# Kernel optimization log

Hardware: AMD Instinct MI355X
Metric: run time of the kernel (lower is better)

Reference implementation:

```python
import jax, jax.numpy as jnp
import numpy as np

SCALES = (3, 9, 17, 33)  # must be odd so padding=s//2 preserves spatial size


def _box_conv(img, s):
    # img: [B,1,H,W]; conv with an all-ones s x s kernel, 'same' padding for odd s
    k = jnp.ones((1, 1, s, s), img.dtype)
    p = s // 2
    return jax.lax.conv_general_dilated(
        img, k, window_strides=(1, 1), padding=[(p, p), (p, p)],
        dimension_numbers=("NCHW", "OIHW", "NCHW"))


def setup_inputs() -> dict:
    key = jax.random.key(0)
    B, C, H, W = 8, 3, 1024, 1024
    x = jax.random.normal(key, (B, C, H, W), dtype=jnp.float32)
    # mimicking sparse path-traced samples
    keep = jax.random.uniform(jax.random.fold_in(key, 1), (B, 1, H, W)) >= 0.3
    x = jnp.where(keep, x, 0.0)
    return {"x": x}


def reference(x):
    # F.conv2d(x, ones(1,3,1,1)/3) == per-pixel mean over the 3 channels
    lum = jnp.mean(x, axis=1, keepdims=True)          # [B,1,H,W]
    nonzero = (lum != 0).astype(lum.dtype)            # [B,1,H,W]
    feats = []
    for s in SCALES:
        count = _box_conv(nonzero, s)                 # number of nonzero pixels in window
        pool = _box_conv(lum, s) / jnp.maximum(count, 1.0)  # mean over nonzero pixels
        feats.append(count / float(s * s))            # percentage of nonzero pixels
        feats.append(pool)
    return jnp.concatenate(feats, axis=1)             # [B, 2*len(SCALES), H, W]
```

## Files before the change

### kernel.cpp

```cpp
#include <hip/hip_runtime.h>


constexpr int THREADS = 256;
constexpr int LOADW   = 256;
constexpr int HALO    = 17;
constexpr int COUT    = 223;
constexpr int RING    = 36;
constexpr int ROWSEG  = 64;

__device__ __forceinline__ void barrier_lds() {
    asm volatile("s_waitcnt lgkmcnt(0)" ::: "memory");
    __builtin_amdgcn_s_barrier();
    __builtin_amdgcn_sched_barrier(0);
}

template<int CTRL, int RM>
__device__ __forceinline__ float dppadd(float v) {
    int sh = __builtin_amdgcn_update_dpp(0, __float_as_int(v), CTRL, RM, 0xF, true);
    return v + __int_as_float(sh);
}

__device__ __forceinline__ float wave_iscan(float v) {
    v = dppadd<0x111, 0xF>(v);
    v = dppadd<0x112, 0xF>(v);
    v = dppadd<0x114, 0xF>(v);
    v = dppadd<0x118, 0xF>(v);
    v = dppadd<0x142, 0xA>(v);
    v = dppadd<0x143, 0xC>(v);
    return v;
}

__global__ __launch_bounds__(THREADS, 3)
void nzfeat_kernel(const float* __restrict__ x, float* __restrict__ out,
                   int B, int H, int W) {
    constexpr int   PP[4]   = {1, 4, 8, 16};
    constexpr float INVA[4] = {1.f/9.f, 1.f/81.f, 1.f/289.f, 1.f/1089.f};

    __shared__ float         ringL[RING][LOADW];
    __shared__ unsigned char ringN[RING][LOADW];
    __shared__ float2        wsum[2][4];

    const int t    = threadIdx.x;
    const int lane = t & 63;
    const int wv   = t >> 6;

    const int x0 = blockIdx.x * COUT;
    const int y0 = blockIdx.y * ROWSEG;
    const int b  = blockIdx.z;

    const int    gx   = x0 - HALO + t;
    const bool   gxok = (gx >= 0) && (gx < W);
    const int    gxc  = min(max(gx, 0), W - 1);
    const size_t HW   = (size_t)H * W;
    const float* xb   = x + (size_t)b * 3 * HW + gxc;

    auto load_row = [&](int r, float& a0, float& a1, float& a2) {
        const int rc = min(max(r, 0), H - 1);
        const float* p = xb + (size_t)rc * W;
        a0 = p[0]; a1 = p[HW]; a2 = p[2 * HW];
    };

    auto slotOf = [&](int r) { return (int)((unsigned)(r + 72) % (unsigned)RING); };
    auto wpos   = [&](int v) { return v >= RING ? v - RING : v; };
    auto wneg   = [&](int v) { return v < 0 ? v + RING : v; };

    auto scan_local = [&](float c0, float c1, float c2, int r, int which) -> float2 {
        float lum = 0.f;
        if (gxok && (unsigned)r < (unsigned)H)
            lum = (c0 + c1 + c2) * (1.0f / 3.0f);
        const bool nzb = (lum != 0.f);
        unsigned long long m = __ballot(nzb);
        int below = __builtin_amdgcn_mbcnt_hi((unsigned)(m >> 32),
                      __builtin_amdgcn_mbcnt_lo((unsigned)m, 0));
        float np = (float)below + (nzb ? 1.f : 0.f);
        float lp = wave_iscan(lum);
        if (lane == 63) wsum[which][wv] = make_float2(lp, np);
        return make_float2(lp, np);
    };

    auto combine_write = [&](float2 A, float2 Bv, int sA, int sB) {
        float oAl = 0.f, oAn = 0.f, oBl = 0.f, oBn = 0.f;
        #pragma unroll
        for (int w2 = 0; w2 < 3; ++w2)
            if (w2 < wv) {
                float2 u = wsum[0][w2]; float2 v = wsum[1][w2];
                oAl += u.x; oAn += u.y; oBl += v.x; oBn += v.y;
            }
        ringL[sA][t] = A.x + oAl;
        ringN[sA][t] = (unsigned char)(int)(A.y + oAn);
        ringL[sB][t] = Bv.x + oBl;
        ringN[sB][t] = (unsigned char)(int)(Bv.y + oBn);
    };

    float a0, a1, a2, b0c, b1c, b2c;
    load_row(y0 - 18, a0, a1, a2);
    load_row(y0 - 17, b0c, b1c, b2c);
    for (int i = 0; i < 17; ++i) {
        const int rA = y0 - 18 + 2 * i;
        float n0, n1, n2, m0, m1, m2;
        load_row(rA + 2, n0, n1, n2);
        load_row(rA + 3, m0, m1, m2);
        float2 A  = scan_local(a0, a1, a2, rA, 0);
        float2 Bv = scan_local(b0c, b1c, b2c, rA + 1, 1);
        barrier_lds();
        combine_write(A, Bv, slotOf(rA), slotOf(rA + 1));
        barrier_lds();
        a0 = n0; a1 = n1; a2 = n2; b0c = m0; b1c = m1; b2c = m2;
    }

    const bool activeCol = (t < COUT) && (x0 + t < W);
    float* outb = out + (size_t)b * 8 * HW + (x0 + t);

    float vl[4], vn[4];
    #pragma unroll
    for (int i = 0; i < 4; ++i) {
        const int p  = PP[i];
        const int d  = 2 * p + 1;
        const int x1 = t + HALO - p - 1;
        float sl = 0.f, sn = 0.f;
        for (int rr = y0 - 1 - p; rr <= y0 - 1 + p; ++rr) {
            const int s = slotOf(rr);
            sl += ringL[s][x1 + d] - ringL[s][x1];
            sn += (float)(unsigned char)(ringN[s][x1 + d] - ringN[s][x1]);
        }
        vl[i] = sl; vn[i] = sn;
    }

    int sy = slotOf(y0);
    for (int k = 0; k < ROWSEG / 2; ++k) {
        const int yk = y0 + 2 * k;
        const int wA = yk + 16;

        float n0, n1, n2, m0, m1, m2;
        load_row(wA + 2, n0, n1, n2);
        load_row(wA + 3, m0, m1, m2);

        float2 A  = scan_local(a0, a1, a2, wA, 0);
        float2 Bv = scan_local(b0c, b1c, b2c, wA + 1, 1);
        barrier_lds();
        combine_write(A, Bv, wpos(sy + 16), wpos(sy + 17));
        barrier_lds();

        #pragma unroll
        for (int i = 0; i < 4; ++i) {
            const int p  = PP[i];
            const int d  = 2 * p + 1;
            const int x1 = t + HALO - p - 1;
            const int sE = wpos(sy + p);
            const int sL = wneg(sy - 1 - p);
            const float hlE = ringL[sE][x1 + d] - ringL[sE][x1];
            const float hnE = (float)(unsigned char)(ringN[sE][x1 + d] - ringN[sE][x1]);
            const float hlL = ringL[sL][x1 + d] - ringL[sL][x1];
            const float hnL = (float)(unsigned char)(ringN[sL][x1 + d] - ringN[sL][x1]);
            vl[i] += hlE - hlL;
            vn[i] += hnE - hnL;
        }
        if (activeCol && yk < H) {
            float* o = outb + (size_t)yk * W;
            #pragma unroll
            for (int i = 0; i < 4; ++i) {
                o[(size_t)(2 * i) * HW]     = vn[i] * INVA[i];
                o[(size_t)(2 * i + 1) * HW] = vl[i] / fmaxf(vn[i], 1.f);
            }
        }

        #pragma unroll
        for (int i = 0; i < 4; ++i) {
            const int p  = PP[i];
            const int d  = 2 * p + 1;
            const int x1 = t + HALO - p - 1;
            const int sE = wpos(sy + p + 1);
            const int sL = wneg(sy - p);
            const float hlE = ringL[sE][x1 + d] - ringL[sE][x1];
            const float hnE = (float)(unsigned char)(ringN[sE][x1 + d] - ringN[sE][x1]);
            const float hlL = ringL[sL][x1 + d] - ringL[sL][x1];
            const float hnL = (float)(unsigned char)(ringN[sL][x1 + d] - ringN[sL][x1]);
            vl[i] += hlE - hlL;
            vn[i] += hnE - hnL;
        }
        if (activeCol && yk + 1 < H) {
            float* o = outb + (size_t)(yk + 1) * W;
            #pragma unroll
            for (int i = 0; i < 4; ++i) {
                o[(size_t)(2 * i) * HW]     = vn[i] * INVA[i];
                o[(size_t)(2 * i + 1) * HW] = vl[i] / fmaxf(vn[i], 1.f);
            }
        }

        sy = wpos(sy + 2);
        a0 = n0; a1 = n1; a2 = n2; b0c = m0; b1c = m1; b2c = m2;
    }
}

extern "C" void kernel_launch(void* const* d_in, const int* in_sizes, int n_in,
                              void* d_out, int out_size, void* d_ws, size_t ws_size,
                              hipStream_t stream) {
    const float* x   = (const float*)d_in[0];
    float*       out = (float*)d_out;

    const int H = 1024, W = 1024;
    const int B = in_sizes[0] / (3 * H * W);

    dim3 grid((W + COUT - 1) / COUT, (H + ROWSEG - 1) / ROWSEG, B);
    nzfeat_kernel<<<grid, dim3(THREADS), 0, stream>>>(x, out, B, H, W);
}
```

Measured before the change: 128.7 us.

## Skew scan and box-sum phases to drop one barrier per row pair

The ring buffer grows from 36 to 38 slots and the per-wave partial sums are double-buffered by parity. This lets the prefix-scan write for the next row pair happen in the same barrier interval as the box-sum reads of the previous pair, removing the second barrier in both loops. The main loop gains an extra drain iteration and extra conditionals. The pool division is also replaced with a hardware reciprocal multiply, which is slightly less accurate.

```diff
diff --git a/kernel.cpp b/kernel.cpp
--- a/kernel.cpp
+++ b/kernel.cpp
@@ -5,7 +5,7 @@
 constexpr int LOADW   = 256;
 constexpr int HALO    = 17;
 constexpr int COUT    = 223;
-constexpr int RING    = 36;
+constexpr int RING    = 38;
 constexpr int ROWSEG  = 64;
 
 __device__ __forceinline__ void barrier_lds() {
@@ -38,7 +38,7 @@
 
     __shared__ float         ringL[RING][LOADW];
     __shared__ unsigned char ringN[RING][LOADW];
-    __shared__ float2        wsum[2][4];
+    __shared__ float2        wsum[2][2][4];
 
     const int t    = threadIdx.x;
     const int lane = t & 63;
@@ -60,11 +60,11 @@
         a0 = p[0]; a1 = p[HW]; a2 = p[2 * HW];
     };
 
-    auto slotOf = [&](int r) { return (int)((unsigned)(r + 72) % (unsigned)RING); };
+    auto slotOf = [&](int r) { return (int)((unsigned)(r + 2 * RING) % (unsigned)RING); };
     auto wpos   = [&](int v) { return v >= RING ? v - RING : v; };
     auto wneg   = [&](int v) { return v < 0 ? v + RING : v; };
 
-    auto scan_local = [&](float c0, float c1, float c2, int r, int which) -> float2 {
+    auto scan_local = [&](float c0, float c1, float c2, int r, int par, int which) -> float2 {
         float lum = 0.f;
         if (gxok && (unsigned)r < (unsigned)H)
             lum = (c0 + c1 + c2) * (1.0f / 3.0f);
@@ -74,16 +74,16 @@
                       __builtin_amdgcn_mbcnt_lo((unsigned)m, 0));
         float np = (float)below + (nzb ? 1.f : 0.f);
         float lp = wave_iscan(lum);
-        if (lane == 63) wsum[which][wv] = make_float2(lp, np);
+        if (lane == 63) wsum[par][which][wv] = make_float2(lp, np);
         return make_float2(lp, np);
     };
 
-    auto combine_write = [&](float2 A, float2 Bv, int sA, int sB) {
+    auto combine_write = [&](int par, float2 A, float2 Bv, int sA, int sB) {
         float oAl = 0.f, oAn = 0.f, oBl = 0.f, oBn = 0.f;
         #pragma unroll
         for (int w2 = 0; w2 < 3; ++w2)
             if (w2 < wv) {
-                float2 u = wsum[0][w2]; float2 v = wsum[1][w2];
+                float2 u = wsum[par][0][w2]; float2 v = wsum[par][1][w2];
                 oAl += u.x; oAn += u.y; oBl += v.x; oBn += v.y;
             }
         ringL[sA][t] = A.x + oAl;
@@ -100,13 +100,13 @@
         float n0, n1, n2, m0, m1, m2;
         load_row(rA + 2, n0, n1, n2);
         load_row(rA + 3, m0, m1, m2);
-        float2 A  = scan_local(a0, a1, a2, rA, 0);
-        float2 Bv = scan_local(b0c, b1c, b2c, rA + 1, 1);
+        float2 A  = scan_local(a0, a1, a2, rA, i & 1, 0);
+        float2 Bv = scan_local(b0c, b1c, b2c, rA + 1, i & 1, 1);
         barrier_lds();
-        combine_write(A, Bv, slotOf(rA), slotOf(rA + 1));
-        barrier_lds();
+        combine_write(i & 1, A, Bv, slotOf(rA), slotOf(rA + 1));
         a0 = n0; a1 = n1; a2 = n2; b0c = m0; b1c = m1; b2c = m2;
     }
+    barrier_lds();
 
     const bool activeCol = (t < COUT) && (x0 + t < W);
     float* outb = out + (size_t)b * 8 * HW + (x0 + t);
@@ -127,68 +127,81 @@
     }
 
     int sy = slotOf(y0);
-    for (int k = 0; k < ROWSEG / 2; ++k) {
-        const int yk = y0 + 2 * k;
-        const int wA = yk + 16;
-
-        float n0, n1, n2, m0, m1, m2;
-        load_row(wA + 2, n0, n1, n2);
-        load_row(wA + 3, m0, m1, m2);
-
-        float2 A  = scan_local(a0, a1, a2, wA, 0);
-        float2 Bv = scan_local(b0c, b1c, b2c, wA + 1, 1);
+    int sw = slotOf(y0 + 16);
+    for (int k = 0; k <= ROWSEG / 2; ++k) {
+        const bool doScan = (k < ROWSEG / 2);
+        float2 A = make_float2(0.f, 0.f), Bv = make_float2(0.f, 0.f);
+        float n0 = 0.f, n1 = 0.f, n2 = 0.f, m0 = 0.f, m1 = 0.f, m2 = 0.f;
+        if (doScan) {
+            const int wA = y0 + 2 * k + 16;
+            if (k < ROWSEG / 2 - 1) {
+                load_row(wA + 2, n0, n1, n2);
+                load_row(wA + 3, m0, m1, m2);
+            }
+            A  = scan_local(a0, a1, a2, wA, k & 1, 0);
+            Bv = scan_local(b0c, b1c, b2c, wA + 1, k & 1, 1);
+        }
         barrier_lds();
-        combine_write(A, Bv, wpos(sy + 16), wpos(sy + 17));
-        barrier_lds();
-
-        #pragma unroll
-        for (int i = 0; i < 4; ++i) {
-            const int p  = PP[i];
-            const int d  = 2 * p + 1;
-            const int x1 = t + HALO - p - 1;
-            const int sE = wpos(sy + p);
-            const int sL = wneg(sy - 1 - p);
-            const float hlE = ringL[sE][x1 + d] - ringL[sE][x1];
-            const float hnE = (float)(unsigned char)(ringN[sE][x1 + d] - ringN[sE][x1]);
-            const float hlL = ringL[sL][x1 + d] - ringL[sL][x1];
-            const float hnL = (float)(unsigned char)(ringN[sL][x1 + d] - ringN[sL][x1]);
-            vl[i] += hlE - hlL;
-            vn[i] += hnE - hnL;
-        }
-        if (activeCol && yk < H) {
-            float* o = outb + (size_t)yk * W;
+        if (doScan) {
+            combine_write(k & 1, A, Bv, sw, wpos(sw + 1));
+            sw = wpos(sw + 2);
+        }
+        if (k >= 1) {
+            const int ye = y0 + 2 * (k - 1);
+
             #pragma unroll
             for (int i = 0; i < 4; ++i) {
-                o[(size_t)(2 * i) * HW]     = vn[i] * INVA[i];
-                o[(size_t)(2 * i + 1) * HW] = vl[i] / fmaxf(vn[i], 1.f);
-            }
-        }
-
-        #pragma unroll
-        for (int i = 0; i < 4; ++i) {
-            const int p  = PP[i];
-            const int d  = 2 * p + 1;
-            const int x1 = t + HALO - p - 1;
-            const int sE = wpos(sy + p + 1);
-            const int sL = wneg(sy - p);
-            const float hlE = ringL[sE][x1 + d] - ringL[sE][x1];
-            const float hnE = (float)(unsigned char)(ringN[sE][x1 + d] - ringN[sE][x1]);
-            const float hlL = ringL[sL][x1 + d] - ringL[sL][x1];
-            const float hnL = (float)(unsigned char)(ringN[sL][x1 + d] - ringN[sL][x1]);
-            vl[i] += hlE - hlL;
-            vn[i] += hnE - hnL;
-        }
-        if (activeCol && yk + 1 < H) {
-            float* o = outb + (size_t)(yk + 1) * W;
+                const int p  = PP[i];
+                const int d  = 2 * p + 1;
+                const int x1 = t + HALO - p - 1;
+                const int sE = wpos(sy + p);
+                const int sL = wneg(sy - 1 - p);
+                const float hlE = ringL[sE][x1 + d] - ringL[sE][x1];
+                const float hnE = (float)(unsigned char)(ringN[sE][x1 + d] - ringN[sE][x1]);
+                const float hlL = ringL[sL][x1 + d] - ringL[sL][x1];
+                const float hnL = (float)(unsigned char)(ringN[sL][x1 + d] - ringN[sL][x1]);
+                vl[i] += hlE - hlL;
+                vn[i] += hnE - hnL;
+            }
+            if (activeCol && ye < H) {
+                float* o = outb + (size_t)ye * W;
+                #pragma unroll
+                for (int i = 0; i < 4; ++i) {
+                    o[(size_t)(2 * i) * HW]     = vn[i] * INVA[i];
+                    o[(size_t)(2 * i + 1) * HW] =
+                        vl[i] * __builtin_amdgcn_rcpf(fmaxf(vn[i], 1.f));
+                }
+            }
+
             #pragma unroll
             for (int i = 0; i < 4; ++i) {
-                o[(size_t)(2 * i) * HW]     = vn[i] * INVA[i];
-                o[(size_t)(2 * i + 1) * HW] = vl[i] / fmaxf(vn[i], 1.f);
-            }
-        }
-
-        sy = wpos(sy + 2);
-        a0 = n0; a1 = n1; a2 = n2; b0c = m0; b1c = m1; b2c = m2;
+                const int p  = PP[i];
+                const int d  = 2 * p + 1;
+                const int x1 = t + HALO - p - 1;
+                const int sE = wpos(sy + p + 1);
+                const int sL = wneg(sy - p);
+                const float hlE = ringL[sE][x1 + d] - ringL[sE][x1];
+                const float hnE = (float)(unsigned char)(ringN[sE][x1 + d] - ringN[sE][x1]);
+                const float hlL = ringL[sL][x1 + d] - ringL[sL][x1];
+                const float hnL = (float)(unsigned char)(ringN[sL][x1 + d] - ringN[sL][x1]);
+                vl[i] += hlE - hlL;
+                vn[i] += hnE - hnL;
+            }
+            if (activeCol && ye + 1 < H) {
+                float* o = outb + (size_t)(ye + 1) * W;
+                #pragma unroll
+                for (int i = 0; i < 4; ++i) {
+                    o[(size_t)(2 * i) * HW]     = vn[i] * INVA[i];
+                    o[(size_t)(2 * i + 1) * HW] =
+                        vl[i] * __builtin_amdgcn_rcpf(fmaxf(vn[i], 1.f));
+                }
+            }
+
+            sy = wpos(sy + 2);
+        }
+        if (k < ROWSEG / 2 - 1) {
+            a0 = n0; a1 = n1; a2 = n2; b0c = m0; b1c = m1; b2c = m2;
+        }
     }
 }
 
```

Result: no change. 128.7 us (+0.0%).
